# Kernel tuning notes

Hardware: AMD Instinct MI355X
Metric: run time of the kernel (lower is better)

The kernel has to match this reference:

```python
import jax, jax.numpy as jnp
import numpy as np

DIM = 2048
N_HEADS = 16
KV_HEADS = 2 * 2  # 4
HEAD_DIM = DIM // N_HEADS  # 128
B, T = 2, 2048


def apply_rope(x, cos, sin):
    # Faithful to the source: x is replaced by its rotated version, then
    # multiplied by (sin + cos). x: [B,H,T,D], cos/sin: [T,D] broadcast.
    x1 = x[..., ::2]
    x2 = x[..., 1::2]
    rot = jnp.stack((-x2, x1), axis=-1).reshape(x.shape)
    return rot * sin + rot * cos


def setup_inputs() -> dict:
    key = jax.random.key(0)
    ks = jax.random.split(key, 8)
    x = jax.random.normal(ks[0], (B, T, DIM), dtype=jnp.float32)
    cos = jax.random.uniform(ks[1], (T, HEAD_DIM), dtype=jnp.float32)
    sin = jax.random.uniform(ks[2], (T, HEAD_DIM), dtype=jnp.float32)
    mask = jnp.tril(jnp.ones((T, T), dtype=bool))  # causal
    s = 1.0 / np.sqrt(DIM)
    Wq = jax.random.normal(ks[3], (DIM, DIM), dtype=jnp.float32) * s
    Wk = jax.random.normal(ks[4], (KV_HEADS * HEAD_DIM, DIM), dtype=jnp.float32) * s
    Wv = jax.random.normal(ks[5], (KV_HEADS * HEAD_DIM, DIM), dtype=jnp.float32) * s
    Wout = jax.random.normal(ks[6], (DIM, DIM), dtype=jnp.float32) * s
    bout = jax.random.normal(ks[7], (DIM,), dtype=jnp.float32) * s
    return {"x": x, "cos": cos, "sin": sin, "mask": mask,
            "Wq": Wq, "Wk": Wk, "Wv": Wv, "Wout": Wout, "bout": bout}


def reference(x, cos, sin, mask, Wq, Wk, Wv, Wout, bout):
    Bb, Tt, C = x.shape
    # projections (torch Linear: x @ W.T)
    q = (x @ Wq.T).reshape(Bb, Tt, N_HEADS, HEAD_DIM).transpose(0, 2, 1, 3)
    k = (x @ Wk.T).reshape(Bb, Tt, KV_HEADS, HEAD_DIM).transpose(0, 2, 1, 3)
    v = (x @ Wv.T).reshape(Bb, Tt, KV_HEADS, HEAD_DIM).transpose(0, 2, 1, 3)
    q = apply_rope(q, cos, sin)
    k = apply_rope(k, cos, sin)
    repeat = N_HEADS // KV_HEADS
    k = jnp.repeat(k, repeat, axis=1)  # [B,H,T,D]
    v = jnp.repeat(v, repeat, axis=1)
    attn = jnp.einsum("bhtd,bhsd->bhts", q, k) / np.sqrt(HEAD_DIM)
    attn = jnp.where(mask, attn, jnp.float32(-1e9))
    probs = jax.nn.softmax(attn, axis=-1)
    out = jnp.einsum("bhts,bhsd->bhtd", probs, v)
    out = out.transpose(0, 2, 1, 3).reshape(Bb, Tt, C)
    return out @ Wout.T + bout
```

## Files before the change

kernel.cpp:

```cpp
#include <hip/hip_runtime.h>
#include <type_traits>

#define DEVI __device__ __forceinline__

typedef unsigned short u16;
typedef unsigned int u32;
typedef float f32x4 __attribute__((ext_vector_type(4)));
typedef __bf16 bf16x8 __attribute__((ext_vector_type(8)));
typedef unsigned short u16x4 __attribute__((ext_vector_type(4)));
typedef unsigned short u16x8 __attribute__((ext_vector_type(8)));
typedef int i32x4 __attribute__((ext_vector_type(4)));
typedef unsigned int u32x2 __attribute__((ext_vector_type(2)));

constexpr int BATCH = 2;
constexpr int T     = 2048;
constexpr int DIM   = 2048;
constexpr int NH    = 16;
constexpr int KVH   = 4;
constexpr int HD    = 128;
constexpr int NQKV  = DIM + 2 * KVH * HD;
constexpr int ROWS  = BATCH * T;
constexpr float SC2 = 0.08838834764831845f * 1.4426950408889634f;

DEVI u16 f2b(float f) {
  u32 u = __float_as_uint(f);
  return (u16)((u + 0x7fffu + ((u >> 16) & 1u)) >> 16);
}
DEVI float b2f(u16 u) { return __uint_as_float(((u32)u) << 16); }

DEVI u32 cvtpk(float lo, float hi) {
  u32 r;
  asm("v_cvt_pk_bf16_f32 %0, %1, %2" : "=v"(r) : "v"(lo), "v"(hi));
  return r;
}

DEVI f32x4 mfma16(bf16x8 a, bf16x8 b, f32x4 c) {
  return __builtin_amdgcn_mfma_f32_16x16x32_bf16(a, b, c, 0, 0, 0);
}
DEVI void gload16(const void* g, void* l) {
  __builtin_amdgcn_global_load_lds((const __attribute__((address_space(1))) void*)g,
                                   (__attribute__((address_space(3))) void*)l, 16, 0, 0);
}

__global__ void cvt_all_kernel(const float* __restrict__ x,
                               const float* __restrict__ Wq, const float* __restrict__ Wk,
                               const float* __restrict__ Wv, const float* __restrict__ Wo,
                               const float* __restrict__ cosp, const float* __restrict__ sinp,
                               u16* __restrict__ xb, u16* __restrict__ wqkv,
                               u16* __restrict__ wout, float* __restrict__ cs)
{
  constexpr int S0 = ROWS * DIM / 4;
  constexpr int S1 = DIM * DIM / 4;
  constexpr int S2 = 512 * DIM / 4;
  constexpr int S3 = 512 * DIM / 4;
  constexpr int S4 = DIM * DIM / 4;
  constexpr int S5 = T * HD / 4;
  int i = blockIdx.x * 256 + threadIdx.x;
  const float* src; u16* dst;
  if (i < S0) { src = x; dst = xb; }
  else if ((i -= S0) < S1) { src = Wq; dst = wqkv; }
  else if ((i -= S1) < S2) { src = Wk; dst = wqkv + DIM * DIM; }
  else if ((i -= S2) < S3) { src = Wv; dst = wqkv + (size_t)(DIM + 512) * DIM; }
  else if ((i -= S3) < S4) { src = Wo; dst = wout; }
  else if ((i -= S4) < S5) {
    float4 c = ((const float4*)cosp)[i];
    float4 s = ((const float4*)sinp)[i];
    float4 o = { c.x + s.x, c.y + s.y, c.z + s.z, c.w + s.w };
    ((float4*)cs)[i] = o;
    return;
  } else return;
  float4 v = ((const float4*)src)[i];
  u16x4 o = { f2b(v.x), f2b(v.y), f2b(v.z), f2b(v.w) };
  ((u16x4*)dst)[i] = o;
}

template<bool BF16OUT, bool BIAS>
__global__ __launch_bounds__(256) void gemm_bt_kernel(
    const u16* __restrict__ A, const u16* __restrict__ W,
    void* __restrict__ Cout, const float* __restrict__ bias,
    int M, int N, int K)
{
  constexpr int BK = 64;
  __shared__ u16 sA[128 * BK];
  __shared__ u16 sB[128 * BK];
  const int nbx = N >> 7;
  const int bx = blockIdx.x % nbx;
  const int by = blockIdx.x / nbx;
  const int m0 = by << 7, n0 = bx << 7;
  const int tid = threadIdx.x;
  const int w = tid >> 6, lane = tid & 63;
  const int wr = w >> 1, wc = w & 1;
  const int lq = lane & 15, lg = lane >> 4;

  f32x4 acc[4][4] = {};

  int srow[4], scb[4];
#pragma unroll
  for (int c = 0; c < 4; ++c) {
    int off = (w * 4 + c) * 1024 + lane * 16;
    srow[c] = off >> 7;
    scb[c]  = (off & 127) ^ ((srow[c] & 7) << 4);
  }

  for (int kt = 0; kt < K; kt += BK) {
#pragma unroll
    for (int c = 0; c < 4; ++c) {
      u16* la = sA + (w * 4 + c) * 512;
      u16* lb = sB + (w * 4 + c) * 512;
      gload16(A + (size_t)(m0 + srow[c]) * K + kt + (scb[c] >> 1), la);
      gload16(W + (size_t)(n0 + srow[c]) * K + kt + (scb[c] >> 1), lb);
    }
    __syncthreads();
#pragma unroll
    for (int ks = 0; ks < 2; ++ks) {
      bf16x8 af[4], bfr[4];
#pragma unroll
      for (int i = 0; i < 4; ++i) {
        int ra = wr * 64 + i * 16 + lq;
        int ca = (ks * 64 + lg * 16) ^ ((ra & 7) << 4);
        af[i] = *(const bf16x8*)((const char*)sA + ra * 128 + ca);
        int rb = wc * 64 + i * 16 + lq;
        int cb = (ks * 64 + lg * 16) ^ ((rb & 7) << 4);
        bfr[i] = *(const bf16x8*)((const char*)sB + rb * 128 + cb);
      }
#pragma unroll
      for (int i = 0; i < 4; ++i)
#pragma unroll
        for (int j = 0; j < 4; ++j)
          acc[i][j] = mfma16(af[i], bfr[j], acc[i][j]);
    }
    __syncthreads();
  }

  const int crow = m0 + wr * 64 + lg * 4;
  const int ccol = n0 + wc * 64 + lq;
#pragma unroll
  for (int j = 0; j < 4; ++j) {
    int col = ccol + j * 16;
    float bv = BIAS ? bias[col] : 0.0f;
#pragma unroll
    for (int i = 0; i < 4; ++i)
#pragma unroll
      for (int r = 0; r < 4; ++r) {
        size_t idx = (size_t)(crow + i * 16 + r) * N + col;
        float v = acc[i][j][r] + bv;
        if (BF16OUT) ((u16*)Cout)[idx] = f2b(v);
        else         ((float*)Cout)[idx] = v;
      }
  }
}

template<int NHEADS, int COLBASE>
__global__ void rope_kernel(const u16* __restrict__ Y, const float* __restrict__ cs,
                            u16* __restrict__ out, float scale)
{
  int pid = blockIdx.x * 256 + threadIdx.x;
  constexpr int TOTAL = ROWS * NHEADS * (HD / 2);
  if (pid >= TOTAL) return;
  int i  = pid & 63;
  int hr = pid >> 6;
  int h  = hr & (NHEADS - 1);
  int r  = hr / NHEADS;
  int t  = r & (T - 1);
  int b  = r >> 11;
  u32 y = *(const u32*)(Y + (size_t)r * NQKV + COLBASE + h * HD + 2 * i);
  float y0 = b2f((u16)(y & 0xffffu));
  float y1 = b2f((u16)(y >> 16));
  const float* cp = cs + t * HD + 2 * i;
  u32 o = (u32)f2b(-y1 * cp[0] * scale) | ((u32)f2b(y0 * cp[1] * scale) << 16);
  *(u32*)(out + (((size_t)(b * NHEADS + h) * T + t) * HD + 2 * i)) = o;
}

__global__ __launch_bounds__(256) void vt_kernel(const u16* __restrict__ Y, u16* __restrict__ vt)
{
  __shared__ u16 tile[64][136];
  const int tid = threadIdx.x;
  const int tc = blockIdx.x & 31;
  const int kh = (blockIdx.x >> 5) & 3;
  const int b  = blockIdx.x >> 7;
  const u16* src = Y + (size_t)(b * T + tc * 64) * NQKV + (DIM + KVH * HD) + kh * HD;
#pragma unroll
  for (int pass = 0; pass < 4; ++pass) {
    int r = pass * 16 + (tid >> 4);
    int c = (tid & 15) * 8;
    *(u16x8*)&tile[r][c] = *(const u16x8*)(src + (size_t)r * NQKV + c);
  }
  __syncthreads();
  const int d = tid >> 1, th = tid & 1;
  u16* dst = vt + ((size_t)((b * KVH + kh) * HD + d) * T) + tc * 64 + th * 32;
#pragma unroll
  for (int j = 0; j < 4; ++j) {
    u16x8 v;
#pragma unroll
    for (int e = 0; e < 8; ++e) v[e] = tile[th * 32 + j * 8 + e][d];
    *(u16x8*)(dst + j * 8) = v;
  }
}

__global__ __launch_bounds__(256, 2) void attn_kernel(
    const u16* __restrict__ Qr, const u16* __restrict__ Kr,
    const u16* __restrict__ Vt, u16* __restrict__ Aout)
{
  __shared__ u16 ldsK[2][64 * 128];
  __shared__ u16 ldsV[2][128 * 64];
  __shared__ u16 ldsP[4][32 * 40];

  const int tid = threadIdx.x;
  const int w = tid >> 6, lane = tid & 63;
  const int lq = lane & 15, lg = lane >> 4;

  const int p  = (blockIdx.x >> 3) & 15;
  const int bh = (blockIdx.x & 7) * 4 + (blockIdx.x >> 7);
  const int b = bh >> 4, h = bh & 15, kh = h >> 2;
  const int qcA = p, qcB = 31 - p;
  const int rowA = qcA * 64 + w * 16;
  const int rowB = qcB * 64 + w * 16;
  const int nst = qcB + 1;

  bf16x8 qf[2][4];
  {
    const u16* QpA = Qr + ((size_t)bh * T + rowA + lq) * HD + lg * 8;
    const u16* QpB = Qr + ((size_t)bh * T + rowB + lq) * HD + lg * 8;
#pragma unroll
    for (int ds = 0; ds < 4; ++ds) {
      qf[0][ds] = *(const bf16x8*)(QpA + ds * 32);
      qf[1][ds] = *(const bf16x8*)(QpB + ds * 32);
    }
  }

  const u16* Kg = Kr + (size_t)(b * KVH + kh) * T * HD;
  const u16* Vg = Vt + (size_t)(b * KVH + kh) * HD * T;

  int kgo[4], klb[4], vgo[4], vlb[4];
  {
    const int vr = lane >> 3, vc = lane & 7;
#pragma unroll
    for (int i = 0; i < 4; ++i) {
      int krow = w * 16 + i * 4 + lg;
      kgo[i] = krow * HD + (((lq * 16) ^ ((krow & 7) << 4)) >> 1);
      klb[i] = (w * 16 + i * 4) * 128;
      int vrow = w * 32 + i * 8 + vr;
      vgo[i] = vrow * T + (((vc * 16) ^ ((vr & 7) << 4)) >> 1);
      vlb[i] = (w * 32 + i * 8) * 64;
    }
  }

  f32x4 accO[2][8] = {};
  float lsum[2] = { 0.f, 0.f };

#pragma unroll
  for (int i = 0; i < 4; ++i) {
    gload16(Kg + kgo[i], &ldsK[0][klb[i]]);
    gload16(Vg + vgo[i], &ldsV[0][vlb[i]]);
  }
  __syncthreads();

  int cur = 0;
  for (int t = 0; t < nst; ++t) {
    if (t + 1 < nst) {
      const u16* Kt  = Kg + (size_t)(t + 1) * 64 * HD;
      const u16* Vts = Vg + (t + 1) * 64;
#pragma unroll
      for (int i = 0; i < 4; ++i) {
        gload16(Kt + kgo[i],  &ldsK[cur ^ 1][klb[i]]);
        gload16(Vts + vgo[i], &ldsV[cur ^ 1][vlb[i]]);
      }
    }
    const int s0 = t << 6;
    const u16* Kb = ldsK[cur];
    const u16* Vb = ldsV[cur];

    auto softmax_qg = [&](f32x4 (&s4)[4], int qidx, bool diag, float& ls,
                          float (&pp)[16]) {
      if (diag) {
#pragma unroll
        for (int si = 0; si < 4; ++si)
#pragma unroll
          for (int r = 0; r < 4; ++r) {
            int s = s0 + si * 16 + lg * 4 + r;
            pp[si * 4 + r] = (s <= qidx) ? __builtin_amdgcn_exp2f(s4[si][r]) : 0.0f;
          }
      } else {
#pragma unroll
        for (int si = 0; si < 4; ++si)
#pragma unroll
          for (int r = 0; r < 4; ++r)
            pp[si * 4 + r] = __builtin_amdgcn_exp2f(s4[si][r]);
      }
      float ps = 0.f;
#pragma unroll
      for (int i2 = 0; i2 < 16; ++i2) ps += pp[i2];
      ps += __shfl_xor(ps, 16);
      ps += __shfl_xor(ps, 32);
      ls += ps;
    };

    auto tile_body = [&](auto hasA_c) {
      constexpr bool HASA = decltype(hasA_c)::value;
      f32x4 aS[2][4] = {};
      __builtin_amdgcn_s_setprio(1);
#pragma unroll
      for (int si = 0; si < 4; ++si)
#pragma unroll
        for (int ds = 0; ds < 4; ++ds) {
          const u16* kp = Kb + (si * 16 + lq) * 128 +
                          (((ds * 64 + lg * 16) ^ ((lq & 7) << 4)) >> 1);
          bf16x8 kf = *(const bf16x8*)kp;
          if constexpr (HASA) aS[0][si] = mfma16(kf, qf[0][ds], aS[0][si]);
          aS[1][si] = mfma16(kf, qf[1][ds], aS[1][si]);
        }
      __builtin_amdgcn_s_setprio(0);

      float pp[2][16];
      if constexpr (HASA)
        softmax_qg(aS[0], rowA + lq, t == qcA, lsum[0], pp[0]);
      softmax_qg(aS[1], rowB + lq, t == qcB, lsum[1], pp[1]);

#pragma unroll
      for (int ks = 0; ks < 2; ++ks) {
        if constexpr (HASA) {
          u16* pw = &ldsP[w][lq * 40];
          u32x2 wa = { cvtpk(pp[0][8 * ks + 0], pp[0][8 * ks + 1]),
                       cvtpk(pp[0][8 * ks + 2], pp[0][8 * ks + 3]) };
          u32x2 wb = { cvtpk(pp[0][8 * ks + 4], pp[0][8 * ks + 5]),
                       cvtpk(pp[0][8 * ks + 6], pp[0][8 * ks + 7]) };
          *(u32x2*)(pw + lg * 4)      = wa;
          *(u32x2*)(pw + 16 + lg * 4) = wb;
        }
        {
          u16* pw = &ldsP[w][(16 + lq) * 40];
          u32x2 wa = { cvtpk(pp[1][8 * ks + 0], pp[1][8 * ks + 1]),
                       cvtpk(pp[1][8 * ks + 2], pp[1][8 * ks + 3]) };
          u32x2 wb = { cvtpk(pp[1][8 * ks + 4], pp[1][8 * ks + 5]),
                       cvtpk(pp[1][8 * ks + 6], pp[1][8 * ks + 7]) };
          *(u32x2*)(pw + lg * 4)      = wa;
          *(u32x2*)(pw + 16 + lg * 4) = wb;
        }
        asm volatile("" ::: "memory");
        bf16x8 pf0, pf1;
        if constexpr (HASA) pf0 = *(const bf16x8*)(&ldsP[w][lq * 40] + lg * 8);
        pf1 = *(const bf16x8*)(&ldsP[w][(16 + lq) * 40] + lg * 8);
        asm volatile("" ::: "memory");
        __builtin_amdgcn_s_setprio(1);
#pragma unroll
        for (int db = 0; db < 8; ++db) {
          const u16* vp = Vb + (db * 16 + lq) * 64 +
                          (((ks * 64 + lg * 16) ^ ((lq & 7) << 4)) >> 1);
          bf16x8 vf = *(const bf16x8*)vp;
          if constexpr (HASA) accO[0][db] = mfma16(vf, pf0, accO[0][db]);
          accO[1][db] = mfma16(vf, pf1, accO[1][db]);
        }
        __builtin_amdgcn_s_setprio(0);
      }
    };

    if (t <= qcA) tile_body(std::integral_constant<bool, true>{});
    else          tile_body(std::integral_constant<bool, false>{});

    __syncthreads();
    cur ^= 1;
  }

#pragma unroll
  for (int qg = 0; qg < 2; ++qg) {
    const int rowX = qg ? rowB : rowA;
    float inv = 1.0f / (qg ? lsum[1] : lsum[0]);
    u16* Ab = Aout + ((size_t)b * T + rowX + lq) * DIM + h * HD;
#pragma unroll
    for (int db = 0; db < 8; ++db) {
      f32x4 a = qg ? accO[1][db] : accO[0][db];
      u32x2 st = { cvtpk(a[0] * inv, a[1] * inv),
                   cvtpk(a[2] * inv, a[3] * inv) };
      *(u32x2*)(Ab + db * 16 + lg * 4) = st;
    }
  }
}

extern "C" void kernel_launch(void* const* d_in, const int* in_sizes, int n_in,
                              void* d_out, int out_size, void* d_ws, size_t ws_size,
                              hipStream_t stream) {
  const float* x    = (const float*)d_in[0];
  const float* cosp = (const float*)d_in[1];
  const float* sinp = (const float*)d_in[2];
  const float* Wq   = (const float*)d_in[4];
  const float* Wk   = (const float*)d_in[5];
  const float* Wv   = (const float*)d_in[6];
  const float* Wo   = (const float*)d_in[7];
  const float* bo   = (const float*)d_in[8];

  char* ws = (char*)d_ws;
  u16*   xb   = (u16*)(ws + 0);
  u16*   wqkv = (u16*)(ws + 16777216);
  u16*   wout = (u16*)(ws + 29360128);
  float* cs   = (float*)(ws + 37748736);
  u16*   yqkv = (u16*)(ws + 38797312);
  u16*   kr   = (u16*)(ws + 63963136);
  u16*   vt   = (u16*)(ws + 68157440);
  u16* qr   = xb;
  u16* aout = yqkv;

  constexpr int CVT_TOTAL = ROWS * DIM / 4 + DIM * DIM / 4 + 512 * DIM / 4 * 2
                          + DIM * DIM / 4 + T * HD / 4;
  cvt_all_kernel<<<(CVT_TOTAL + 255) / 256, 256, 0, stream>>>(
      x, Wq, Wk, Wv, Wo, cosp, sinp, xb, wqkv, wout, cs);

  gemm_bt_kernel<true, false><<<(ROWS / 128) * (NQKV / 128), 256, 0, stream>>>(
      xb, wqkv, yqkv, nullptr, ROWS, NQKV, DIM);

  rope_kernel<NH, 0><<<ROWS * NH * 64 / 256, 256, 0, stream>>>(yqkv, cs, qr, SC2);
  rope_kernel<KVH, DIM><<<ROWS * KVH * 64 / 256, 256, 0, stream>>>(yqkv, cs, kr, 1.0f);
  vt_kernel<<<BATCH * KVH * (T / 64), 256, 0, stream>>>(yqkv, vt);

  attn_kernel<<<BATCH * NH * 16, 256, 0, stream>>>(qr, kr, vt, aout);

  gemm_bt_kernel<false, true><<<(ROWS / 128) * (DIM / 128), 256, 0, stream>>>(
      aout, wout, d_out, bo, ROWS, DIM, DIM);
}
```

Measured before the change: 201.9 us.

## Load V directly from global into registers, merge rope kernels, defer row-sum reduction

The attention kernel drops the double-buffered LDS staging for V and reads V^T fragments straight from global memory into registers for the PV MFMAs. This frees LDS so occupancy can rise, with launch bounds going from 2 to 3 blocks per CU. The per-tile cross-lane shuffle reduction of the softmax sum moves to a single reduction in the epilogue, and the two rope launches are fused into one. The trade is that V loads are no longer prefetched ahead of use, so global-memory latency may sit on the critical path before the PV MFMAs.

Result: slower. 512.8 us (+154.0%).

```diff
diff --git a/kernel.cpp b/kernel.cpp
--- a/kernel.cpp
+++ b/kernel.cpp
@@ -9,7 +9,6 @@
 typedef __bf16 bf16x8 __attribute__((ext_vector_type(8)));
 typedef unsigned short u16x4 __attribute__((ext_vector_type(4)));
 typedef unsigned short u16x8 __attribute__((ext_vector_type(8)));
-typedef int i32x4 __attribute__((ext_vector_type(4)));
 typedef unsigned int u32x2 __attribute__((ext_vector_type(2)));
 
 constexpr int BATCH = 2;
@@ -151,12 +150,9 @@
 }
 
 template<int NHEADS, int COLBASE>
-__global__ void rope_kernel(const u16* __restrict__ Y, const float* __restrict__ cs,
-                            u16* __restrict__ out, float scale)
-{
-  int pid = blockIdx.x * 256 + threadIdx.x;
-  constexpr int TOTAL = ROWS * NHEADS * (HD / 2);
-  if (pid >= TOTAL) return;
+DEVI void rope_one(const u16* __restrict__ Y, const float* __restrict__ cs,
+                   u16* __restrict__ out, int pid, float scale)
+{
   int i  = pid & 63;
   int hr = pid >> 6;
   int h  = hr & (NHEADS - 1);
@@ -171,6 +167,15 @@
   *(u32*)(out + (((size_t)(b * NHEADS + h) * T + t) * HD + 2 * i)) = o;
 }
 
+__global__ void rope_qk_kernel(const u16* __restrict__ Y, const float* __restrict__ cs,
+                               u16* __restrict__ qr, u16* __restrict__ kr)
+{
+  int pid = blockIdx.x * 256 + threadIdx.x;
+  constexpr int NQ = ROWS * NH * (HD / 2);
+  if (pid < NQ) rope_one<NH, 0>(Y, cs, qr, pid, SC2);
+  else          rope_one<KVH, DIM>(Y, cs, kr, pid - NQ, 1.0f);
+}
+
 __global__ __launch_bounds__(256) void vt_kernel(const u16* __restrict__ Y, u16* __restrict__ vt)
 {
   __shared__ u16 tile[64][136];
@@ -197,12 +202,11 @@
   }
 }
 
-__global__ __launch_bounds__(256, 2) void attn_kernel(
+__global__ __launch_bounds__(256, 3) void attn_kernel(
     const u16* __restrict__ Qr, const u16* __restrict__ Kr,
     const u16* __restrict__ Vt, u16* __restrict__ Aout)
 {
   __shared__ u16 ldsK[2][64 * 128];
-  __shared__ u16 ldsV[2][128 * 64];
   __shared__ u16 ldsP[4][32 * 40];
 
   const int tid = threadIdx.x;
@@ -231,44 +235,30 @@
   const u16* Kg = Kr + (size_t)(b * KVH + kh) * T * HD;
   const u16* Vg = Vt + (size_t)(b * KVH + kh) * HD * T;
 
-  int kgo[4], klb[4], vgo[4], vlb[4];
-  {
-    const int vr = lane >> 3, vc = lane & 7;
-#pragma unroll
-    for (int i = 0; i < 4; ++i) {
-      int krow = w * 16 + i * 4 + lg;
-      kgo[i] = krow * HD + (((lq * 16) ^ ((krow & 7) << 4)) >> 1);
-      klb[i] = (w * 16 + i * 4) * 128;
-      int vrow = w * 32 + i * 8 + vr;
-      vgo[i] = vrow * T + (((vc * 16) ^ ((vr & 7) << 4)) >> 1);
-      vlb[i] = (w * 32 + i * 8) * 64;
-    }
+  int kgo[4], klb[4];
+#pragma unroll
+  for (int i = 0; i < 4; ++i) {
+    int krow = w * 16 + i * 4 + lg;
+    kgo[i] = krow * HD + (((lq * 16) ^ ((krow & 7) << 4)) >> 1);
+    klb[i] = (w * 16 + i * 4) * 128;
   }
 
   f32x4 accO[2][8] = {};
   float lsum[2] = { 0.f, 0.f };
 
 #pragma unroll
-  for (int i = 0; i < 4; ++i) {
-    gload16(Kg + kgo[i], &ldsK[0][klb[i]]);
-    gload16(Vg + vgo[i], &ldsV[0][vlb[i]]);
-  }
+  for (int i = 0; i < 4; ++i) gload16(Kg + kgo[i], &ldsK[0][klb[i]]);
   __syncthreads();
 
   int cur = 0;
   for (int t = 0; t < nst; ++t) {
     if (t + 1 < nst) {
-      const u16* Kt  = Kg + (size_t)(t + 1) * 64 * HD;
-      const u16* Vts = Vg + (t + 1) * 64;
-#pragma unroll
-      for (int i = 0; i < 4; ++i) {
-        gload16(Kt + kgo[i],  &ldsK[cur ^ 1][klb[i]]);
-        gload16(Vts + vgo[i], &ldsV[cur ^ 1][vlb[i]]);
-      }
+      const u16* Kt = Kg + (size_t)(t + 1) * 64 * HD;
+#pragma unroll
+      for (int i = 0; i < 4; ++i) gload16(Kt + kgo[i], &ldsK[cur ^ 1][klb[i]]);
     }
     const int s0 = t << 6;
     const u16* Kb = ldsK[cur];
-    const u16* Vb = ldsV[cur];
 
     auto softmax_qg = [&](f32x4 (&s4)[4], int qidx, bool diag, float& ls,
                           float (&pp)[16]) {
@@ -290,8 +280,6 @@
       float ps = 0.f;
 #pragma unroll
       for (int i2 = 0; i2 < 16; ++i2) ps += pp[i2];
-      ps += __shfl_xor(ps, 16);
-      ps += __shfl_xor(ps, 32);
       ls += ps;
     };
 
@@ -318,6 +306,11 @@
 
 #pragma unroll
       for (int ks = 0; ks < 2; ++ks) {
+        bf16x8 vf[8];
+#pragma unroll
+        for (int db = 0; db < 8; ++db)
+          vf[db] = *(const bf16x8*)(Vg + (size_t)(db * 16 + lq) * T + s0 + ks * 32 + lg * 8);
+
         if constexpr (HASA) {
           u16* pw = &ldsP[w][lq * 40];
           u32x2 wa = { cvtpk(pp[0][8 * ks + 0], pp[0][8 * ks + 1]),
@@ -344,11 +337,8 @@
         __builtin_amdgcn_s_setprio(1);
 #pragma unroll
         for (int db = 0; db < 8; ++db) {
-          const u16* vp = Vb + (db * 16 + lq) * 64 +
-                          (((ks * 64 + lg * 16) ^ ((lq & 7) << 4)) >> 1);
-          bf16x8 vf = *(const bf16x8*)vp;
-          if constexpr (HASA) accO[0][db] = mfma16(vf, pf0, accO[0][db]);
-          accO[1][db] = mfma16(vf, pf1, accO[1][db]);
+          if constexpr (HASA) accO[0][db] = mfma16(vf[db], pf0, accO[0][db]);
+          accO[1][db] = mfma16(vf[db], pf1, accO[1][db]);
         }
         __builtin_amdgcn_s_setprio(0);
       }
@@ -364,7 +354,10 @@
 #pragma unroll
   for (int qg = 0; qg < 2; ++qg) {
     const int rowX = qg ? rowB : rowA;
-    float inv = 1.0f / (qg ? lsum[1] : lsum[0]);
+    float l = qg ? lsum[1] : lsum[0];
+    l += __shfl_xor(l, 16);
+    l += __shfl_xor(l, 32);
+    float inv = 1.0f / l;
     u16* Ab = Aout + ((size_t)b * T + rowX + lq) * DIM + h * HD;
 #pragma unroll
     for (int db = 0; db < 8; ++db) {
@@ -407,8 +400,7 @@
   gemm_bt_kernel<true, false><<<(ROWS / 128) * (NQKV / 128), 256, 0, stream>>>(
       xb, wqkv, yqkv, nullptr, ROWS, NQKV, DIM);
 
-  rope_kernel<NH, 0><<<ROWS * NH * 64 / 256, 256, 0, stream>>>(yqkv, cs, qr, SC2);
-  rope_kernel<KVH, DIM><<<ROWS * KVH * 64 / 256, 256, 0, stream>>>(yqkv, cs, kr, 1.0f);
+  rope_qk_kernel<<<ROWS * (NH + KVH) * 64 / 256, 256, 0, stream>>>(yqkv, cs, qr, kr);
   vt_kernel<<<BATCH * KVH * (T / 64), 256, 0, stream>>>(yqkv, vt);
 
   attn_kernel<<<BATCH * NH * 16, 256, 0, stream>>>(qr, kr, vt, aout);
```

## Use 256x128 triple-buffered GEMM for output projection, merge rope kernels, defer row-sum shuffles

Applied to the files above, without the earlier changes.

Adds a new 512-thread GEMM kernel with 256x128 tiles and a three-stage shared-memory pipeline, with loads split across the two k-substeps, and uses it for the output projection. The two rope launches are merged into one kernel. The attention row-sum cross-lane shuffles move out of the per-tile loop and run once at the end. The larger tile yields only 256 blocks for the out-projection, which may underfill the CUs, and the high shared-memory use limits occupancy to one block per CU.

Measured after the change: 213.0 us. 5.5% more time.

```diff
diff --git a/kernel.cpp b/kernel.cpp
--- a/kernel.cpp
+++ b/kernel.cpp
@@ -9,7 +9,6 @@
 typedef __bf16 bf16x8 __attribute__((ext_vector_type(8)));
 typedef unsigned short u16x4 __attribute__((ext_vector_type(4)));
 typedef unsigned short u16x8 __attribute__((ext_vector_type(8)));
-typedef int i32x4 __attribute__((ext_vector_type(4)));
 typedef unsigned int u32x2 __attribute__((ext_vector_type(2)));
 
 constexpr int BATCH = 2;
@@ -150,13 +149,142 @@
   }
 }
 
+template<bool BF16OUT, bool BIAS>
+__global__ __launch_bounds__(512, 1) void gemm256_kernel(
+    const u16* __restrict__ A, const u16* __restrict__ W,
+    void* __restrict__ Cout, const float* __restrict__ bias,
+    int M, int N, int K)
+{
+  __shared__ u16 sA[3][256 * 64];
+  __shared__ u16 sB[3][128 * 64];
+  const int tid = threadIdx.x;
+  const int wid = tid >> 6, lane = tid & 63;
+  const int wr = wid >> 1, wc = wid & 1;
+  const int lq = lane & 15, lg = lane >> 4;
+
+  const int nbx = N >> 7;
+  const int by = blockIdx.x / nbx, bx = blockIdx.x % nbx;
+  const int m0 = by << 8, n0 = bx << 7;
+
+  const int srow8 = lane >> 3;
+  const int scol  = ((lane & 7) ^ srow8) << 3;
+  size_t aoff[4]; int aldst[4];
+#pragma unroll
+  for (int i = 0; i < 4; ++i) {
+    int row = (wid * 4 + i) * 8 + srow8;
+    aoff[i] = (size_t)(m0 + row) * K + scol;
+    aldst[i] = (wid * 4 + i) * 512;
+  }
+  size_t boff[2]; int bldst[2];
+#pragma unroll
+  for (int i = 0; i < 2; ++i) {
+    int row = (wid * 2 + i) * 8 + srow8;
+    boff[i] = (size_t)(n0 + row) * K + scol;
+    bldst[i] = (wid * 2 + i) * 512;
+  }
+
+  const int arow = (wr * 64 + lq) * 128;
+  const int brow = (wc * 64 + lq) * 128;
+  int cks[2];
+#pragma unroll
+  for (int ks = 0; ks < 2; ++ks) cks[ks] = (ks * 64 + lg * 16) ^ ((lq & 7) << 4);
+
+  f32x4 acc[4][4] = {};
+
+#pragma unroll
+  for (int i = 0; i < 4; ++i) gload16(A + aoff[i], &sA[0][aldst[i]]);
+#pragma unroll
+  for (int i = 0; i < 2; ++i) gload16(W + boff[i], &sB[0][bldst[i]]);
+#pragma unroll
+  for (int i = 0; i < 4; ++i) gload16(A + aoff[i] + 64, &sA[1][aldst[i]]);
+#pragma unroll
+  for (int i = 0; i < 2; ++i) gload16(W + boff[i] + 64, &sB[1][bldst[i]]);
+  asm volatile("s_waitcnt vmcnt(6)" ::: "memory");
+  __builtin_amdgcn_s_barrier();
+
+  const int NT = K >> 6;
+  int cur = 0, pre = 2;
+  for (int t = 0; t < NT; ++t) {
+    const char* sAc = (const char*)sA[cur];
+    const char* sBc = (const char*)sB[cur];
+    u16* sAp = sA[pre];
+    u16* sBp = sB[pre];
+    const bool st = (t + 2 < NT);
+    const u16* Ap = A + (size_t)(t + 2) * 64;
+    const u16* Wp = W + (size_t)(t + 2) * 64;
+
+    bf16x8 aF[4], bF[4];
+
+    if (st) {
+      gload16(Ap + aoff[0], sAp + aldst[0]);
+      gload16(Ap + aoff[1], sAp + aldst[1]);
+      gload16(Wp + boff[0], sBp + bldst[0]);
+    }
+#pragma unroll
+    for (int m = 0; m < 4; ++m) aF[m] = *(const bf16x8*)(sAc + arow + m * 2048 + cks[0]);
+#pragma unroll
+    for (int n = 0; n < 4; ++n) bF[n] = *(const bf16x8*)(sBc + brow + n * 2048 + cks[0]);
+    __builtin_amdgcn_s_barrier();
+    asm volatile("s_waitcnt lgkmcnt(0)" ::: "memory");
+    __builtin_amdgcn_sched_barrier(0);
+    __builtin_amdgcn_s_setprio(1);
+#pragma unroll
+    for (int m = 0; m < 4; ++m)
+#pragma unroll
+      for (int n = 0; n < 4; ++n)
+        acc[m][n] = mfma16(aF[m], bF[n], acc[m][n]);
+    __builtin_amdgcn_s_setprio(0);
+    __builtin_amdgcn_s_barrier();
+
+    if (st) {
+      gload16(Ap + aoff[2], sAp + aldst[2]);
+      gload16(Ap + aoff[3], sAp + aldst[3]);
+      gload16(Wp + boff[1], sBp + bldst[1]);
+    }
+#pragma unroll
+    for (int m = 0; m < 4; ++m) aF[m] = *(const bf16x8*)(sAc + arow + m * 2048 + cks[1]);
+#pragma unroll
+    for (int n = 0; n < 4; ++n) bF[n] = *(const bf16x8*)(sBc + brow + n * 2048 + cks[1]);
+    __builtin_amdgcn_s_barrier();
+    asm volatile("s_waitcnt lgkmcnt(0)" ::: "memory");
+    __builtin_amdgcn_sched_barrier(0);
+    __builtin_amdgcn_s_setprio(1);
+#pragma unroll
+    for (int m = 0; m < 4; ++m)
+#pragma unroll
+      for (int n = 0; n < 4; ++n)
+        acc[m][n] = mfma16(aF[m], bF[n], acc[m][n]);
+    __builtin_amdgcn_s_setprio(0);
+    if (st)              asm volatile("s_waitcnt vmcnt(6)" ::: "memory");
+    else if (t + 1 < NT) asm volatile("s_waitcnt vmcnt(0)" ::: "memory");
+    __builtin_amdgcn_s_barrier();
+
+    cur = (cur == 2) ? 0 : cur + 1;
+    pre = (pre == 2) ? 0 : pre + 1;
+  }
+
+  const int crow = m0 + wr * 64 + lg * 4;
+  const int ccol = n0 + wc * 64 + lq;
+#pragma unroll
+  for (int n = 0; n < 4; ++n) {
+    int col = ccol + n * 16;
+    float bv = BIAS ? bias[col] : 0.0f;
+#pragma unroll
+    for (int m = 0; m < 4; ++m)
+#pragma unroll
+      for (int r = 0; r < 4; ++r) {
+        size_t idx = (size_t)(crow + m * 16 + r) * N + col;
+        float v = acc[m][n][r] + bv;
+        if (BF16OUT) ((u16*)Cout)[idx] = f2b(v);
+        else         ((float*)Cout)[idx] = v;
+      }
+  }
+}
+
 template<int NHEADS, int COLBASE>
-__global__ void rope_kernel(const u16* __restrict__ Y, const float* __restrict__ cs,
-                            u16* __restrict__ out, float scale)
-{
-  int pid = blockIdx.x * 256 + threadIdx.x;
-  constexpr int TOTAL = ROWS * NHEADS * (HD / 2);
-  if (pid >= TOTAL) return;
+DEVI void rope_one(const u16* __restrict__ Y, const float* __restrict__ cs,
+                   u16* __restrict__ out, int pid, float scale)
+{
   int i  = pid & 63;
   int hr = pid >> 6;
   int h  = hr & (NHEADS - 1);
@@ -171,6 +299,15 @@
   *(u32*)(out + (((size_t)(b * NHEADS + h) * T + t) * HD + 2 * i)) = o;
 }
 
+__global__ void rope_qk_kernel(const u16* __restrict__ Y, const float* __restrict__ cs,
+                               u16* __restrict__ qr, u16* __restrict__ kr)
+{
+  int pid = blockIdx.x * 256 + threadIdx.x;
+  constexpr int NQ = ROWS * NH * (HD / 2);
+  if (pid < NQ) rope_one<NH, 0>(Y, cs, qr, pid, SC2);
+  else          rope_one<KVH, DIM>(Y, cs, kr, pid - NQ, 1.0f);
+}
+
 __global__ __launch_bounds__(256) void vt_kernel(const u16* __restrict__ Y, u16* __restrict__ vt)
 {
   __shared__ u16 tile[64][136];
@@ -290,8 +427,6 @@
       float ps = 0.f;
 #pragma unroll
       for (int i2 = 0; i2 < 16; ++i2) ps += pp[i2];
-      ps += __shfl_xor(ps, 16);
-      ps += __shfl_xor(ps, 32);
       ls += ps;
     };
 
@@ -364,7 +499,10 @@
 #pragma unroll
   for (int qg = 0; qg < 2; ++qg) {
     const int rowX = qg ? rowB : rowA;
-    float inv = 1.0f / (qg ? lsum[1] : lsum[0]);
+    float l = qg ? lsum[1] : lsum[0];
+    l += __shfl_xor(l, 16);
+    l += __shfl_xor(l, 32);
+    float inv = 1.0f / l;
     u16* Ab = Aout + ((size_t)b * T + rowX + lq) * DIM + h * HD;
 #pragma unroll
     for (int db = 0; db < 8; ++db) {
@@ -407,12 +545,11 @@
   gemm_bt_kernel<true, false><<<(ROWS / 128) * (NQKV / 128), 256, 0, stream>>>(
       xb, wqkv, yqkv, nullptr, ROWS, NQKV, DIM);
 
-  rope_kernel<NH, 0><<<ROWS * NH * 64 / 256, 256, 0, stream>>>(yqkv, cs, qr, SC2);
-  rope_kernel<KVH, DIM><<<ROWS * KVH * 64 / 256, 256, 0, stream>>>(yqkv, cs, kr, 1.0f);
+  rope_qk_kernel<<<ROWS * (NH + KVH) * 64 / 256, 256, 0, stream>>>(yqkv, cs, qr, kr);
   vt_kernel<<<BATCH * KVH * (T / 64), 256, 0, stream>>>(yqkv, vt);
 
   attn_kernel<<<BATCH * NH * 16, 256, 0, stream>>>(qr, kr, vt, aout);
 
-  gemm_bt_kernel<false, true><<<(ROWS / 128) * (DIM / 128), 256, 0, stream>>>(
+  gemm256_kernel<false, true><<<(ROWS / 256) * (DIM / 128), 512, 0, stream>>>(
       aout, wout, d_out, bo, ROWS, DIM, DIM);
 }
```

## Fuse Q rope into attention prologue and defer row-sum reduction

Applied to the files above, without the earlier changes.

Removes the separate Q rope kernel: the attention kernel now reads raw Q from the QKV projection output, applies the rotation and cos/sin scaling in registers, and packs bf16 fragments directly. This drops a full write and re-read of the Q tensor plus one launch. The per-tile cross-lane shuffle reduction of the softmax row sum is also moved to the epilogue, reducing work inside the inner loop. The attention output buffer is moved to the x buffer, which is no longer needed, since the QKV buffer must now stay live.

New measurement: 193.0 us. 4.4% less time.

```diff
diff --git a/kernel.cpp b/kernel.cpp
--- a/kernel.cpp
+++ b/kernel.cpp
@@ -9,7 +9,6 @@
 typedef __bf16 bf16x8 __attribute__((ext_vector_type(8)));
 typedef unsigned short u16x4 __attribute__((ext_vector_type(4)));
 typedef unsigned short u16x8 __attribute__((ext_vector_type(8)));
-typedef int i32x4 __attribute__((ext_vector_type(4)));
 typedef unsigned int u32x2 __attribute__((ext_vector_type(2)));
 
 constexpr int BATCH = 2;
@@ -150,25 +149,22 @@
   }
 }
 
-template<int NHEADS, int COLBASE>
-__global__ void rope_kernel(const u16* __restrict__ Y, const float* __restrict__ cs,
-                            u16* __restrict__ out, float scale)
+__global__ void rope_k_kernel(const u16* __restrict__ Y, const float* __restrict__ cs,
+                              u16* __restrict__ kr)
 {
   int pid = blockIdx.x * 256 + threadIdx.x;
-  constexpr int TOTAL = ROWS * NHEADS * (HD / 2);
-  if (pid >= TOTAL) return;
   int i  = pid & 63;
   int hr = pid >> 6;
-  int h  = hr & (NHEADS - 1);
-  int r  = hr / NHEADS;
+  int h  = hr & (KVH - 1);
+  int r  = hr / KVH;
   int t  = r & (T - 1);
   int b  = r >> 11;
-  u32 y = *(const u32*)(Y + (size_t)r * NQKV + COLBASE + h * HD + 2 * i);
+  u32 y = *(const u32*)(Y + (size_t)r * NQKV + DIM + h * HD + 2 * i);
   float y0 = b2f((u16)(y & 0xffffu));
   float y1 = b2f((u16)(y >> 16));
   const float* cp = cs + t * HD + 2 * i;
-  u32 o = (u32)f2b(-y1 * cp[0] * scale) | ((u32)f2b(y0 * cp[1] * scale) << 16);
-  *(u32*)(out + (((size_t)(b * NHEADS + h) * T + t) * HD + 2 * i)) = o;
+  u32 o = (u32)f2b(-y1 * cp[0]) | ((u32)f2b(y0 * cp[1]) << 16);
+  *(u32*)(kr + (((size_t)(b * KVH + h) * T + t) * HD + 2 * i)) = o;
 }
 
 __global__ __launch_bounds__(256) void vt_kernel(const u16* __restrict__ Y, u16* __restrict__ vt)
@@ -198,8 +194,9 @@
 }
 
 __global__ __launch_bounds__(256, 2) void attn_kernel(
-    const u16* __restrict__ Qr, const u16* __restrict__ Kr,
-    const u16* __restrict__ Vt, u16* __restrict__ Aout)
+    const u16* __restrict__ Y, const float* __restrict__ cs,
+    const u16* __restrict__ Kr, const u16* __restrict__ Vt,
+    u16* __restrict__ Aout)
 {
   __shared__ u16 ldsK[2][64 * 128];
   __shared__ u16 ldsV[2][128 * 64];
@@ -218,13 +215,22 @@
   const int nst = qcB + 1;
 
   bf16x8 qf[2][4];
-  {
-    const u16* QpA = Qr + ((size_t)bh * T + rowA + lq) * HD + lg * 8;
-    const u16* QpB = Qr + ((size_t)bh * T + rowB + lq) * HD + lg * 8;
+#pragma unroll
+  for (int qg = 0; qg < 2; ++qg) {
+    const int rowX = qg ? rowB : rowA;
+    const u16* yp = Y + ((size_t)(b * T + rowX + lq)) * NQKV + h * HD + lg * 8;
+    const float* cp = cs + (rowX + lq) * HD + lg * 8;
 #pragma unroll
     for (int ds = 0; ds < 4; ++ds) {
-      qf[0][ds] = *(const bf16x8*)(QpA + ds * 32);
-      qf[1][ds] = *(const bf16x8*)(QpB + ds * 32);
+      u16x8 y = *(const u16x8*)(yp + ds * 32);
+      float4 c0 = *(const float4*)(cp + ds * 32);
+      float4 c1 = *(const float4*)(cp + ds * 32 + 4);
+      u16x8 o;
+      o[0] = f2b(-b2f(y[1]) * c0.x * SC2); o[1] = f2b(b2f(y[0]) * c0.y * SC2);
+      o[2] = f2b(-b2f(y[3]) * c0.z * SC2); o[3] = f2b(b2f(y[2]) * c0.w * SC2);
+      o[4] = f2b(-b2f(y[5]) * c1.x * SC2); o[5] = f2b(b2f(y[4]) * c1.y * SC2);
+      o[6] = f2b(-b2f(y[7]) * c1.z * SC2); o[7] = f2b(b2f(y[6]) * c1.w * SC2);
+      qf[qg][ds] = *(bf16x8*)&o;
     }
   }
 
@@ -290,8 +296,6 @@
       float ps = 0.f;
 #pragma unroll
       for (int i2 = 0; i2 < 16; ++i2) ps += pp[i2];
-      ps += __shfl_xor(ps, 16);
-      ps += __shfl_xor(ps, 32);
       ls += ps;
     };
 
@@ -364,7 +368,10 @@
 #pragma unroll
   for (int qg = 0; qg < 2; ++qg) {
     const int rowX = qg ? rowB : rowA;
-    float inv = 1.0f / (qg ? lsum[1] : lsum[0]);
+    float l = qg ? lsum[1] : lsum[0];
+    l += __shfl_xor(l, 16);
+    l += __shfl_xor(l, 32);
+    float inv = 1.0f / l;
     u16* Ab = Aout + ((size_t)b * T + rowX + lq) * DIM + h * HD;
 #pragma unroll
     for (int db = 0; db < 8; ++db) {
@@ -396,8 +403,7 @@
   u16*   yqkv = (u16*)(ws + 38797312);
   u16*   kr   = (u16*)(ws + 63963136);
   u16*   vt   = (u16*)(ws + 68157440);
-  u16* qr   = xb;
-  u16* aout = yqkv;
+  u16* aout = xb;
 
   constexpr int CVT_TOTAL = ROWS * DIM / 4 + DIM * DIM / 4 + 512 * DIM / 4 * 2
                           + DIM * DIM / 4 + T * HD / 4;
@@ -407,11 +413,10 @@
   gemm_bt_kernel<true, false><<<(ROWS / 128) * (NQKV / 128), 256, 0, stream>>>(
       xb, wqkv, yqkv, nullptr, ROWS, NQKV, DIM);
 
-  rope_kernel<NH, 0><<<ROWS * NH * 64 / 256, 256, 0, stream>>>(yqkv, cs, qr, SC2);
-  rope_kernel<KVH, DIM><<<ROWS * KVH * 64 / 256, 256, 0, stream>>>(yqkv, cs, kr, 1.0f);
+  rope_k_kernel<<<ROWS * KVH * 64 / 256, 256, 0, stream>>>(yqkv, cs, kr);
   vt_kernel<<<BATCH * KVH * (T / 64), 256, 0, stream>>>(yqkv, vt);
 
-  attn_kernel<<<BATCH * NH * 16, 256, 0, stream>>>(qr, kr, vt, aout);
+  attn_kernel<<<BATCH * NH * 16, 256, 0, stream>>>(yqkv, cs, kr, vt, aout);
 
   gemm_bt_kernel<false, true><<<(ROWS / 128) * (DIM / 128), 256, 0, stream>>>(
       aout, wout, d_out, bo, ROWS, DIM, DIM);
```
